# Optimization experiments

Measured on AMD Instinct MI355X. Metric: run time of the kernel, lower is better.

The kernel has to match this reference:

```python
import jax, jax.numpy as jnp
import numpy as np

NUM_HEADS = 16
KEY_DIM = 64
B, S, D = 2, 2048, 1024


def setup_inputs() -> dict:
    key = jax.random.key(0)
    ks = jax.random.split(key, 5)
    scale = 1.0 / np.sqrt(D)
    return {
        "x": jax.random.normal(ks[0], (B, S, D), dtype=jnp.float32),
        "Wq": jax.random.normal(ks[1], (D, NUM_HEADS * KEY_DIM), dtype=jnp.float32) * scale,
        "Wk": jax.random.normal(ks[2], (D, NUM_HEADS * KEY_DIM), dtype=jnp.float32) * scale,
        "Wv": jax.random.normal(ks[3], (D, NUM_HEADS * KEY_DIM), dtype=jnp.float32) * scale,
        "Wo": jax.random.normal(ks[4], (NUM_HEADS * KEY_DIM, D), dtype=jnp.float32) * scale,
    }


def reference(x, Wq, Wk, Wv, Wo):
    b, s, d = x.shape
    h, kd = NUM_HEADS, KEY_DIM
    # QKV projections -> [B, H, S, Kd]
    q = (x @ Wq).reshape(b, s, h, kd).transpose(0, 2, 1, 3)
    k = (x @ Wk).reshape(b, s, h, kd).transpose(0, 2, 1, 3)
    v = (x @ Wv).reshape(b, s, h, kd).transpose(0, 2, 1, 3)
    # scaled dot-product attention, full [B,H,S,S] scores (faithful to source)
    logits = jnp.einsum("bhqd,bhkd->bhqk", q, k) / jnp.sqrt(jnp.float32(kd))
    attn = jax.nn.softmax(logits, axis=-1)
    out = jnp.einsum("bhqk,bhkd->bhqd", attn, v)  # [B,H,S,Kd]
    out = out.transpose(0, 2, 1, 3).reshape(b, s, h * kd)
    return out @ Wo
```

## Files before the change

kernel.cpp:

```cpp
#include <hip/hip_runtime.h>


typedef __attribute__((ext_vector_type(8))) short short8;
typedef __attribute__((ext_vector_type(4))) float f32x4;

#define M_ROWS 4096
#define N_COLS 1024
#define K_DIM  1024
#define SEQ    2048

#define QSCALE 0.18033688011111772f

#if defined(__has_builtin)
#if __has_builtin(__builtin_amdgcn_exp2f)
#define EXP2(x) __builtin_amdgcn_exp2f(x)
#endif
#endif
#ifndef EXP2
#define EXP2(x) exp2f(x)
#endif

#define WAITCNT_VM8 0x0F78
#define WAITCNT_VM4 0x0F74

__device__ inline unsigned short f2bf(float f) {
  unsigned int u = __float_as_uint(f);
  u += 0x7fffu + ((u >> 16) & 1u);
  return (unsigned short)(u >> 16);
}

__device__ inline unsigned int pack2bf(float a, float b) {
  unsigned int ua = __float_as_uint(a); ua += 0x7fffu + ((ua >> 16) & 1u);
  unsigned int ub = __float_as_uint(b); ub += 0x7fffu + ((ub >> 16) & 1u);
  return (ua >> 16) | (ub & 0xffff0000u);
}

__device__ inline unsigned int cvtpk(float lo, float hi) {
  unsigned int r;
  asm("v_cvt_pk_bf16_f32 %0, %1, %2" : "=v"(r) : "v"(lo), "v"(hi));
  return r;
}

__device__ inline void swap32(unsigned int& a, unsigned int& b) {
  asm("v_permlane32_swap_b32 %0, %1" : "+v"(a), "+v"(b));
}
__device__ inline void swap16(unsigned int& a, unsigned int& b) {
  asm("v_permlane16_swap_b32 %0, %1" : "+v"(a), "+v"(b));
}

__device__ inline void async_load16(const unsigned short* gptr, unsigned short* lptr) {
  __builtin_amdgcn_global_load_lds(
      (const __attribute__((address_space(1))) unsigned int*)gptr,
      (__attribute__((address_space(3))) unsigned int*)lptr, 16, 0, 0);
}

__global__ void detect_kernel(const unsigned short* __restrict__ x, int* __restrict__ flag) {
  __shared__ int bad;
  if (threadIdx.x == 0) bad = 0;
  __syncthreads();
  for (int i = threadIdx.x; i < 1024; i += 256) {
    float f = __uint_as_float((unsigned int)x[i] << 16);
    float a = fabsf(f);
    if (!(a < 1e4f)) atomicOr(&bad, 1);
  }
  __syncthreads();
  if (threadIdx.x == 0) *flag = bad ? 0 : 1;
}

__global__ void convert_kernel(const void* __restrict__ src, unsigned short* __restrict__ dst,
                               int n4, const int* __restrict__ flag) {
  const int isbf = *flag;
  const int stride = gridDim.x * blockDim.x;
  for (int i = blockIdx.x * blockDim.x + threadIdx.x; i < n4; i += stride) {
    if (isbf) {
      ((uint2*)dst)[i] = ((const uint2*)src)[i];
    } else {
      float4 v = ((const float4*)src)[i];
      ushort4 o;
      o.x = f2bf(v.x); o.y = f2bf(v.y); o.z = f2bf(v.z); o.w = f2bf(v.w);
      ((ushort4*)dst)[i] = o;
    }
  }
}

__global__ __launch_bounds__(256) void convert_wT4_kernel(
    const void* __restrict__ s0, const void* __restrict__ s1,
    const void* __restrict__ s2, const void* __restrict__ s3,
    unsigned short* __restrict__ d0, unsigned short* __restrict__ d1,
    unsigned short* __restrict__ d2, unsigned short* __restrict__ d3,
    const int* __restrict__ flag) {
  __shared__ unsigned short t[32][33];
  const int z = blockIdx.z;
  const void* src = (z == 0) ? s0 : (z == 1) ? s1 : (z == 2) ? s2 : s3;
  unsigned short* dst = (z == 0) ? d0 : (z == 1) ? d1 : (z == 2) ? d2 : d3;
  const int tid = threadIdx.x;
  const int r0 = blockIdx.y * 32, c0 = blockIdx.x * 32;
  const int kr = tid >> 3, nc = (tid & 7) * 4;
  if (*flag) {
    const unsigned short* W = (const unsigned short*)src;
    uint2 v = *(const uint2*)(W + (size_t)(r0 + kr) * K_DIM + c0 + nc);
    t[kr][nc] = v.x & 0xffff; t[kr][nc + 1] = v.x >> 16;
    t[kr][nc + 2] = v.y & 0xffff; t[kr][nc + 3] = v.y >> 16;
  } else {
    const float* W = (const float*)src;
    float4 v = *(const float4*)(W + (size_t)(r0 + kr) * K_DIM + c0 + nc);
    t[kr][nc] = f2bf(v.x); t[kr][nc + 1] = f2bf(v.y);
    t[kr][nc + 2] = f2bf(v.z); t[kr][nc + 3] = f2bf(v.w);
  }
  __syncthreads();
  const int nr = tid >> 3, kc = (tid & 7) * 4;
  uint2 w;
  w.x = (unsigned int)t[kc][nr] | ((unsigned int)t[kc + 1][nr] << 16);
  w.y = (unsigned int)t[kc + 2][nr] | ((unsigned int)t[kc + 3][nr] << 16);
  *(uint2*)(dst + (size_t)(c0 + nr) * K_DIM + r0 + kc) = w;
}

#define GEMM_DMA(Aptr, Bptr, KTOT, KB, BUF)                                       \
  _Pragma("unroll") for (int r = 0; r < 2; ++r) {                                 \
    int s = r * 256 + wave * 64 + lane;                                           \
    int row = s >> 2, c = s & 3;                                                  \
    int g = c ^ ((row ^ (row >> 2)) & 3);                                         \
    async_load16((Aptr) + (size_t)(m0 + row) * (KTOT) + (KB) + g * 8,             \
                 &As[BUF][(size_t)(r * 256 + wave * 64) * 8]);                    \
    async_load16((Bptr) + (size_t)(n0 + row) * (KTOT) + (KB) + g * 8,             \
                 &Bs[BUF][(size_t)(r * 256 + wave * 64) * 8]);                    \
  }

#define GEMM_MAIN_LOOP(Aptr, Bptr, KTOT)                                          \
  f32x4 acc[4][4];                                                                \
  _Pragma("unroll") for (int i = 0; i < 4; ++i)                                   \
  _Pragma("unroll") for (int j = 0; j < 4; ++j)                                   \
      acc[i][j] = (f32x4){0.f, 0.f, 0.f, 0.f};                                    \
  const int xr = (l15 ^ (l15 >> 2)) & 3;                                          \
  GEMM_DMA(Aptr, Bptr, KTOT, 0, 0)                                                \
  for (int kb = 0; kb < (KTOT); kb += 32) {                                       \
    const int pp = (kb >> 5) & 1;                                                 \
    const int kbn = (kb + 32) & ((KTOT) - 1);                                     \
    GEMM_DMA(Aptr, Bptr, KTOT, kbn, pp ^ 1)                                       \
    __builtin_amdgcn_s_waitcnt(WAITCNT_VM4);                                      \
    __syncthreads();                                                              \
    short8 am[4], bn[4];                                                          \
    _Pragma("unroll") for (int i = 0; i < 4; ++i) {                               \
      int arow = wr * 64 + i * 16 + l15;                                          \
      int brow = wc * 64 + i * 16 + l15;                                          \
      int cc = quad ^ xr;                                                         \
      am[i] = *(const short8*)(&As[pp][arow * 32 + cc * 8]);                      \
      bn[i] = *(const short8*)(&Bs[pp][brow * 32 + cc * 8]);                      \
    }                                                                             \
    _Pragma("unroll") for (int i = 0; i < 4; ++i)                                 \
    _Pragma("unroll") for (int j = 0; j < 4; ++j)                                 \
        acc[i][j] = __builtin_amdgcn_mfma_f32_16x16x32_bf16(am[i], bn[j],         \
                                                            acc[i][j], 0, 0, 0); \
    __syncthreads();                                                              \
  }

__global__ __launch_bounds__(256, 3) void qkv_gemm_kernel(
    const unsigned short* __restrict__ Xb,
    const unsigned short* __restrict__ Wqt,
    const unsigned short* __restrict__ Wkt,
    const unsigned short* __restrict__ Wvt,
    unsigned short* __restrict__ Qb,
    unsigned short* __restrict__ Kb,
    unsigned short* __restrict__ Vt) {
  __shared__ __align__(16) unsigned short As[2][128 * 32];
  __shared__ __align__(16) unsigned short Bs[2][128 * 32];
  const int tid = threadIdx.x;
  const int wave = tid >> 6, lane = tid & 63;
  const int quad = lane >> 4, l15 = lane & 15;
  const int wr = wave >> 1, wc = wave & 1;
  const int m0 = blockIdx.x * 128;
  const int n0 = blockIdx.y * 128;
  const int wsel = blockIdx.z;
  const unsigned short* __restrict__ Bt =
      (wsel == 0) ? Wqt : ((wsel == 1) ? Wkt : Wvt);

  GEMM_MAIN_LOOP(Xb, Bt, K_DIM)

#pragma unroll
  for (int i = 0; i < 4; ++i) {
#pragma unroll
    for (int j = 0; j < 4; ++j) {
      int mbase = m0 + wr * 64 + i * 16 + quad * 4;
      int n = n0 + wc * 64 + j * 16 + l15;
      int h = n >> 6, d = n & 63;
      if (wsel == 2) {
        int b_ = mbase >> 11, s = mbase & 2047;
        uint2 w;
        w.x = cvtpk(acc[i][j][0], acc[i][j][1]);
        w.y = cvtpk(acc[i][j][2], acc[i][j][3]);
        *(uint2*)(Vt + ((size_t)(b_ * 16 + h) * 64 + d) * SEQ + s) = w;
      } else {
#pragma unroll
        for (int r = 0; r < 4; ++r) {
          int m = mbase + r;
          int b_ = m >> 11, s = m & 2047;
          float val = acc[i][j][r];
          if (wsel == 0)
            Qb[((size_t)(b_ * 16 + h) * SEQ + s) * 64 + d] = f2bf(val * QSCALE);
          else
            Kb[((size_t)(b_ * 16 + h) * SEQ + s) * 64 + d] = f2bf(val);
        }
      }
    }
  }
}

__global__ __launch_bounds__(256, 2) void flash_kernel(
    const unsigned short* __restrict__ Qb,
    const unsigned short* __restrict__ Kb,
    const unsigned short* __restrict__ Vt,
    unsigned short* __restrict__ Ob) {
  __shared__ __align__(16) unsigned short Klds[2][128 * 64];
  __shared__ __align__(16) unsigned short Vlds[2][64 * 128];
  const int tid = threadIdx.x;
  const int wave = tid >> 6, lane = tid & 63;
  const int quad = lane >> 4, l15 = lane & 15;
  const int gid = blockIdx.x;
  const int bh = gid & 31;
  const int qidx = gid >> 5;
  const int qbase = qidx * 128 + wave * 32;

  const unsigned short* __restrict__ Qp = Qb + (size_t)bh * SEQ * 64;
  const unsigned short* __restrict__ Kp = Kb + (size_t)bh * SEQ * 64;
  const unsigned short* __restrict__ Vp = Vt + (size_t)bh * 64 * SEQ;

  short8 qf[2][2];
#pragma unroll
  for (int g = 0; g < 2; ++g)
#pragma unroll
    for (int h = 0; h < 2; ++h)
      qf[g][h] = *(const short8*)(Qp + (size_t)(qbase + g * 16 + l15) * 64 + h * 32 + quad * 8);

  f32x4 O[2][4];
#pragma unroll
  for (int g = 0; g < 2; ++g)
#pragma unroll
    for (int t = 0; t < 4; ++t) O[g][t] = (f32x4){0.f, 0.f, 0.f, 0.f};
  float l_i[2] = {0.f, 0.f};

#define FLASH_DMA(KB, BUF)                                                     \
  _Pragma("unroll") for (int r = 0; r < 4; ++r) {                              \
    int s = r * 256 + tid;                                                     \
    int krow = s >> 3, kc = s & 7;                                             \
    int kg = kc ^ (krow & 7);                                                  \
    async_load16(Kp + (size_t)((KB) + krow) * 64 + kg * 8,                     \
                 &Klds[BUF][(size_t)(r * 256 + wave * 64) * 8]);               \
    int vrow = s >> 4, vc = s & 15;                                            \
    int vg = vc ^ (vrow & 15);                                                 \
    async_load16(Vp + (size_t)vrow * SEQ + (KB) + vg * 8,                      \
                 &Vlds[BUF][(size_t)(r * 256 + wave * 64) * 8]);               \
  }

#define QK_READ(t)                                                             \
  int row = (t) * 16 + l15;                                                    \
  int c0 = quad ^ (row & 7), c1 = (quad + 4) ^ (row & 7);                      \
  short8 k0 = *(const short8*)(&Klds[p][row * 64 + c0 * 8]);                   \
  short8 k1 = *(const short8*)(&Klds[p][row * 64 + c1 * 8]);

#define SOFTMAX_G(SRC, PB, G)                                                  \
  {                                                                            \
    float rs = 0.f;                                                            \
    unsigned int wx[8], wy[8];                                                 \
    _Pragma("unroll") for (int t = 0; t < 8; ++t) {                            \
      float p0 = EXP2(SRC[t][0]);                                              \
      float p1 = EXP2(SRC[t][1]);                                              \
      float p2 = EXP2(SRC[t][2]);                                              \
      float p3 = EXP2(SRC[t][3]);                                              \
      rs += (p0 + p1) + (p2 + p3);                                             \
      wx[t] = cvtpk(p0, p1);                                                   \
      wy[t] = cvtpk(p2, p3);                                                   \
    }                                                                          \
    l_i[G] += rs;                                                              \
    _Pragma("unroll") for (int m = 0; m < 4; ++m) {                            \
      unsigned int a = wx[2 * m], c = wx[2 * m + 1];                           \
      unsigned int b = wy[2 * m], d = wy[2 * m + 1];                           \
      swap32(a, c); swap16(a, c);                \
      swap32(b, d); swap16(b, d);                \
      union { short8 s; unsigned int u[4]; } P;                                \
      P.u[0] = a; P.u[1] = b; P.u[2] = c; P.u[3] = d;                          \
      PB[m] = P.s;                                                             \
    }                                                                          \
  }

#define PV_G(PB, G)                                                            \
  _Pragma("unroll") for (int td = 0; td < 4; ++td) {                           \
    int vrow = td * 16 + l15;                                                  \
    _Pragma("unroll") for (int m = 0; m < 4; ++m) {                            \
      short8 vf = *(const short8*)(&Vlds[p][vrow * 128 +                       \
                                           (((m * 4 + quad) ^ l15) * 8)]);     \
      O[G][td] = __builtin_amdgcn_mfma_f32_16x16x32_bf16(vf, PB[m],            \
                                                         O[G][td], 0, 0, 0);   \
    }                                                                          \
  }

  FLASH_DMA(0, 0)

  for (int kb = 0; kb < SEQ; kb += 128) {
    const int p = (kb >> 7) & 1;
    const int kbn = (kb + 128) & (SEQ - 1);
    FLASH_DMA(kbn, p ^ 1)
    __builtin_amdgcn_s_waitcnt(WAITCNT_VM8);
    __syncthreads();

    f32x4 sT0[8], sT1[8];
    __builtin_amdgcn_s_setprio(1);
#pragma unroll
    for (int t = 0; t < 8; ++t) {
      QK_READ(t)
      sT0[t] = __builtin_amdgcn_mfma_f32_16x16x32_bf16(k0, qf[0][0],
               (f32x4){0.f, 0.f, 0.f, 0.f}, 0, 0, 0);
      sT0[t] = __builtin_amdgcn_mfma_f32_16x16x32_bf16(k1, qf[0][1], sT0[t], 0, 0, 0);
    }
    __builtin_amdgcn_s_setprio(0);

#pragma unroll
    for (int t = 0; t < 8; ++t) {
      QK_READ(t)
      sT1[t] = __builtin_amdgcn_mfma_f32_16x16x32_bf16(k0, qf[1][0],
               (f32x4){0.f, 0.f, 0.f, 0.f}, 0, 0, 0);
      sT1[t] = __builtin_amdgcn_mfma_f32_16x16x32_bf16(k1, qf[1][1], sT1[t], 0, 0, 0);
    }
    short8 pb0[4];
    SOFTMAX_G(sT0, pb0, 0)

    PV_G(pb0, 0)
    short8 pb1[4];
    SOFTMAX_G(sT1, pb1, 1)

    PV_G(pb1, 1)

    __syncthreads();
  }

#pragma unroll
  for (int g = 0; g < 2; ++g) {
    l_i[g] += __shfl_xor(l_i[g], 16);
    l_i[g] += __shfl_xor(l_i[g], 32);
  }

  const int b_ = bh >> 4, h = bh & 15;
#pragma unroll
  for (int g = 0; g < 2; ++g) {
    const float inv = 1.f / l_i[g];
    unsigned short* orow = Ob + ((size_t)(b_ * SEQ) + qbase + g * 16 + l15) * N_COLS + h * 64;
#pragma unroll
    for (int t = 0; t < 4; ++t) {
      uint2 w;
      w.x = cvtpk(O[g][t][0] * inv, O[g][t][1] * inv);
      w.y = cvtpk(O[g][t][2] * inv, O[g][t][3] * inv);
      *(uint2*)(orow + t * 16 + quad * 4) = w;
    }
  }
#undef FLASH_DMA
#undef QK_READ
#undef SOFTMAX_G
#undef PV_G
}

__global__ __launch_bounds__(256, 3) void out_gemm_kernel(
    const unsigned short* __restrict__ Ob,
    const unsigned short* __restrict__ Wot,
    void* __restrict__ out,
    const int* __restrict__ flag) {
  __shared__ __align__(16) unsigned short As[2][128 * 32];
  __shared__ __align__(16) unsigned short Bs[2][128 * 32];
  const int tid = threadIdx.x;
  const int wave = tid >> 6, lane = tid & 63;
  const int quad = lane >> 4, l15 = lane & 15;
  const int wr = wave >> 1, wc = wave & 1;
  const int m0 = blockIdx.x * 128;
  const int n0 = blockIdx.y * 128;
  const int isbf = *flag;

  GEMM_MAIN_LOOP(Ob, Wot, N_COLS)

#pragma unroll
  for (int i = 0; i < 4; ++i) {
#pragma unroll
    for (int j = 0; j < 4; ++j) {
      int mbase = m0 + wr * 64 + i * 16 + quad * 4;
      int n = n0 + wc * 64 + j * 16 + l15;
#pragma unroll
      for (int r = 0; r < 4; ++r) {
        float val = acc[i][j][r];
        if (isbf) ((unsigned short*)out)[(size_t)(mbase + r) * K_DIM + n] = f2bf(val);
        else      ((float*)out)[(size_t)(mbase + r) * K_DIM + n] = val;
      }
    }
  }
}

extern "C" void kernel_launch(void* const* d_in, const int* in_sizes, int n_in,
                              void* d_out, int out_size, void* d_ws, size_t ws_size,
                              hipStream_t stream) {
  const void* x  = d_in[0];
  const void* wq = d_in[1];
  const void* wk = d_in[2];
  const void* wv = d_in[3];
  const void* wo = d_in[4];

  char* ws = (char*)d_ws;
  size_t off = 0;
  int* flag = (int*)(ws + off);                 off += 256;
  unsigned short* xb  = (unsigned short*)(ws + off); off += (size_t)M_ROWS * K_DIM * 2;
  unsigned short* wqt = (unsigned short*)(ws + off); off += (size_t)K_DIM * N_COLS * 2;
  unsigned short* wkt = (unsigned short*)(ws + off); off += (size_t)K_DIM * N_COLS * 2;
  unsigned short* wvt = (unsigned short*)(ws + off); off += (size_t)K_DIM * N_COLS * 2;
  unsigned short* wot = (unsigned short*)(ws + off); off += (size_t)N_COLS * K_DIM * 2;
  unsigned short* Qb  = (unsigned short*)(ws + off); off += (size_t)M_ROWS * 1024 * 2;
  unsigned short* Kb  = (unsigned short*)(ws + off); off += (size_t)M_ROWS * 1024 * 2;
  unsigned short* Vtb = (unsigned short*)(ws + off); off += (size_t)M_ROWS * 1024 * 2;
  unsigned short* Ob  = (unsigned short*)(ws + off); off += (size_t)M_ROWS * N_COLS * 2;
  (void)ws_size; (void)in_sizes; (void)n_in; (void)out_size;

  detect_kernel<<<1, 256, 0, stream>>>((const unsigned short*)x, flag);

  convert_kernel<<<2048, 256, 0, stream>>>(x, xb, (M_ROWS * K_DIM) / 4, flag);
  convert_wT4_kernel<<<dim3(32, 32, 4), 256, 0, stream>>>(wq, wk, wv, wo,
                                                          wqt, wkt, wvt, wot, flag);

  qkv_gemm_kernel<<<dim3(32, 8, 3), 256, 0, stream>>>(xb, wqt, wkt, wvt, Qb, Kb, Vtb);
  flash_kernel<<<512, 256, 0, stream>>>(Qb, Kb, Vtb, Ob);
  out_gemm_kernel<<<dim3(32, 8), 256, 0, stream>>>(Ob, wot, d_out, flag);
}
```

Before: 187.5 us.

## Merge detect/convert kernels and triple-buffer GEMM LDS pipeline

Folds the dtype-detection and the input and weight conversion kernels into one launch, with each wave detecting bf16-vs-fp32 inline instead of reading a flag from workspace. This removes two kernel launches and the serial dependency on a single-block detect kernel. The GEMM main loop moves from double to triple buffering: it prefetches two stages ahead and drops the trailing barrier, so there is one __syncthreads per K step instead of two. LDS per block grows by half, which may lower occupancy at 3 blocks per CU, and every wave now repeats the detection reads.

```diff
diff --git a/kernel.cpp b/kernel.cpp
--- a/kernel.cpp
+++ b/kernel.cpp
@@ -29,12 +29,6 @@
   return (unsigned short)(u >> 16);
 }
 
-__device__ inline unsigned int pack2bf(float a, float b) {
-  unsigned int ua = __float_as_uint(a); ua += 0x7fffu + ((ua >> 16) & 1u);
-  unsigned int ub = __float_as_uint(b); ub += 0x7fffu + ((ub >> 16) & 1u);
-  return (ua >> 16) | (ub & 0xffff0000u);
-}
-
 __device__ inline unsigned int cvtpk(float lo, float hi) {
   unsigned int r;
   asm("v_cvt_pk_bf16_f32 %0, %1, %2" : "=v"(r) : "v"(lo), "v"(hi));
@@ -54,49 +48,51 @@
       (__attribute__((address_space(3))) unsigned int*)lptr, 16, 0, 0);
 }
 
-__global__ void detect_kernel(const unsigned short* __restrict__ x, int* __restrict__ flag) {
-  __shared__ int bad;
-  if (threadIdx.x == 0) bad = 0;
-  __syncthreads();
-  for (int i = threadIdx.x; i < 1024; i += 256) {
-    float f = __uint_as_float((unsigned int)x[i] << 16);
-    float a = fabsf(f);
-    if (!(a < 1e4f)) atomicOr(&bad, 1);
-  }
-  __syncthreads();
-  if (threadIdx.x == 0) *flag = bad ? 0 : 1;
-}
-
-__global__ void convert_kernel(const void* __restrict__ src, unsigned short* __restrict__ dst,
-                               int n4, const int* __restrict__ flag) {
-  const int isbf = *flag;
-  const int stride = gridDim.x * blockDim.x;
-  for (int i = blockIdx.x * blockDim.x + threadIdx.x; i < n4; i += stride) {
-    if (isbf) {
-      ((uint2*)dst)[i] = ((const uint2*)src)[i];
-    } else {
-      float4 v = ((const float4*)src)[i];
-      ushort4 o;
-      o.x = f2bf(v.x); o.y = f2bf(v.y); o.z = f2bf(v.z); o.w = f2bf(v.w);
-      ((ushort4*)dst)[i] = o;
-    }
-  }
-}
-
-__global__ __launch_bounds__(256) void convert_wT4_kernel(
+__device__ inline int wave_is_bf16(const unsigned short* __restrict__ x) {
+  const int lane = threadIdx.x & 63;
+  int bad = 0;
+#pragma unroll
+  for (int i = 0; i < 16; ++i) {
+    float f = __uint_as_float((unsigned int)x[lane + i * 64] << 16);
+    if (!(fabsf(f) < 1e4f)) bad = 1;
+  }
+  return __any(bad) ? 0 : 1;
+}
+
+__global__ __launch_bounds__(256) void convert_all_kernel(
+    const void* __restrict__ xsrc,
     const void* __restrict__ s0, const void* __restrict__ s1,
     const void* __restrict__ s2, const void* __restrict__ s3,
+    unsigned short* __restrict__ xb,
     unsigned short* __restrict__ d0, unsigned short* __restrict__ d1,
-    unsigned short* __restrict__ d2, unsigned short* __restrict__ d3,
-    const int* __restrict__ flag) {
+    unsigned short* __restrict__ d2, unsigned short* __restrict__ d3) {
   __shared__ unsigned short t[32][33];
   const int z = blockIdx.z;
+  const int isbf = wave_is_bf16((const unsigned short*)xsrc);
+  const int tid = threadIdx.x;
+
+  if (z == 4) {
+    const int n4 = (M_ROWS * K_DIM) / 4;
+    const int start = (blockIdx.y * 32 + blockIdx.x) * 256 + tid;
+    const int stride = 1024 * 256;
+    for (int i = start; i < n4; i += stride) {
+      if (isbf) {
+        ((uint2*)xb)[i] = ((const uint2*)xsrc)[i];
+      } else {
+        float4 v = ((const float4*)xsrc)[i];
+        ushort4 o;
+        o.x = f2bf(v.x); o.y = f2bf(v.y); o.z = f2bf(v.z); o.w = f2bf(v.w);
+        ((ushort4*)xb)[i] = o;
+      }
+    }
+    return;
+  }
+
   const void* src = (z == 0) ? s0 : (z == 1) ? s1 : (z == 2) ? s2 : s3;
   unsigned short* dst = (z == 0) ? d0 : (z == 1) ? d1 : (z == 2) ? d2 : d3;
-  const int tid = threadIdx.x;
   const int r0 = blockIdx.y * 32, c0 = blockIdx.x * 32;
   const int kr = tid >> 3, nc = (tid & 7) * 4;
-  if (*flag) {
+  if (isbf) {
     const unsigned short* W = (const unsigned short*)src;
     uint2 v = *(const uint2*)(W + (size_t)(r0 + kr) * K_DIM + c0 + nc);
     t[kr][nc] = v.x & 0xffff; t[kr][nc + 1] = v.x >> 16;
@@ -133,25 +129,27 @@
       acc[i][j] = (f32x4){0.f, 0.f, 0.f, 0.f};                                    \
   const int xr = (l15 ^ (l15 >> 2)) & 3;                                          \
   GEMM_DMA(Aptr, Bptr, KTOT, 0, 0)                                                \
+  GEMM_DMA(Aptr, Bptr, KTOT, 32, 1)                                               \
+  int cur = 0;                                                                    \
   for (int kb = 0; kb < (KTOT); kb += 32) {                                       \
-    const int pp = (kb >> 5) & 1;                                                 \
-    const int kbn = (kb + 32) & ((KTOT) - 1);                                     \
-    GEMM_DMA(Aptr, Bptr, KTOT, kbn, pp ^ 1)                                       \
     __builtin_amdgcn_s_waitcnt(WAITCNT_VM4);                                      \
     __syncthreads();                                                              \
+    const int kb2 = (kb + 64) & ((KTOT) - 1);                                     \
+    const int nx2 = (cur == 0) ? 2 : (cur - 1);                    \
+    GEMM_DMA(Aptr, Bptr, KTOT, kb2, nx2)                                          \
     short8 am[4], bn[4];                                                          \
     _Pragma("unroll") for (int i = 0; i < 4; ++i) {                               \
       int arow = wr * 64 + i * 16 + l15;                                          \
       int brow = wc * 64 + i * 16 + l15;                                          \
       int cc = quad ^ xr;                                                         \
-      am[i] = *(const short8*)(&As[pp][arow * 32 + cc * 8]);                      \
-      bn[i] = *(const short8*)(&Bs[pp][brow * 32 + cc * 8]);                      \
+      am[i] = *(const short8*)(&As[cur][arow * 32 + cc * 8]);                     \
+      bn[i] = *(const short8*)(&Bs[cur][brow * 32 + cc * 8]);                     \
     }                                                                             \
     _Pragma("unroll") for (int i = 0; i < 4; ++i)                                 \
     _Pragma("unroll") for (int j = 0; j < 4; ++j)                                 \
         acc[i][j] = __builtin_amdgcn_mfma_f32_16x16x32_bf16(am[i], bn[j],         \
                                                             acc[i][j], 0, 0, 0); \
-    __syncthreads();                                                              \
+    cur = (cur == 2) ? 0 : cur + 1;                                               \
   }
 
 __global__ __launch_bounds__(256, 3) void qkv_gemm_kernel(
@@ -162,8 +160,8 @@
     unsigned short* __restrict__ Qb,
     unsigned short* __restrict__ Kb,
     unsigned short* __restrict__ Vt) {
-  __shared__ __align__(16) unsigned short As[2][128 * 32];
-  __shared__ __align__(16) unsigned short Bs[2][128 * 32];
+  __shared__ __align__(16) unsigned short As[3][128 * 32];
+  __shared__ __align__(16) unsigned short Bs[3][128 * 32];
   const int tid = threadIdx.x;
   const int wave = tid >> 6, lane = tid & 63;
   const int quad = lane >> 4, l15 = lane & 15;
@@ -361,16 +359,16 @@
     const unsigned short* __restrict__ Ob,
     const unsigned short* __restrict__ Wot,
     void* __restrict__ out,
-    const int* __restrict__ flag) {
-  __shared__ __align__(16) unsigned short As[2][128 * 32];
-  __shared__ __align__(16) unsigned short Bs[2][128 * 32];
+    const unsigned short* __restrict__ xdet) {
+  __shared__ __align__(16) unsigned short As[3][128 * 32];
+  __shared__ __align__(16) unsigned short Bs[3][128 * 32];
   const int tid = threadIdx.x;
   const int wave = tid >> 6, lane = tid & 63;
   const int quad = lane >> 4, l15 = lane & 15;
   const int wr = wave >> 1, wc = wave & 1;
   const int m0 = blockIdx.x * 128;
   const int n0 = blockIdx.y * 128;
-  const int isbf = *flag;
+  const int isbf = wave_is_bf16(xdet);
 
   GEMM_MAIN_LOOP(Ob, Wot, N_COLS)
 
@@ -401,7 +399,6 @@
 
   char* ws = (char*)d_ws;
   size_t off = 0;
-  int* flag = (int*)(ws + off);                 off += 256;
   unsigned short* xb  = (unsigned short*)(ws + off); off += (size_t)M_ROWS * K_DIM * 2;
   unsigned short* wqt = (unsigned short*)(ws + off); off += (size_t)K_DIM * N_COLS * 2;
   unsigned short* wkt = (unsigned short*)(ws + off); off += (size_t)K_DIM * N_COLS * 2;
@@ -413,13 +410,10 @@
   unsigned short* Ob  = (unsigned short*)(ws + off); off += (size_t)M_ROWS * N_COLS * 2;
   (void)ws_size; (void)in_sizes; (void)n_in; (void)out_size;
 
-  detect_kernel<<<1, 256, 0, stream>>>((const unsigned short*)x, flag);
-
-  convert_kernel<<<2048, 256, 0, stream>>>(x, xb, (M_ROWS * K_DIM) / 4, flag);
-  convert_wT4_kernel<<<dim3(32, 32, 4), 256, 0, stream>>>(wq, wk, wv, wo,
-                                                          wqt, wkt, wvt, wot, flag);
-
+  convert_all_kernel<<<dim3(32, 32, 5), 256, 0, stream>>>(x, wq, wk, wv, wo,
+                                                          xb, wqt, wkt, wvt, wot);
   qkv_gemm_kernel<<<dim3(32, 8, 3), 256, 0, stream>>>(xb, wqt, wkt, wvt, Qb, Kb, Vtb);
   flash_kernel<<<512, 256, 0, stream>>>(Qb, Kb, Vtb, Ob);
-  out_gemm_kernel<<<dim3(32, 8), 256, 0, stream>>>(Ob, wot, d_out, flag);
-}
+  out_gemm_kernel<<<dim3(32, 8), 256, 0, stream>>>(Ob, wot, d_out,
+                                                   (const unsigned short*)x);
+}
```

After: 191.0 us. No clear change (+1.9%).
